# Kernel optimization log

Hardware: AMD Instinct MI355X
Metric: run time of the kernel (lower is better)

The kernel has to match this reference:

```python
import jax, jax.numpy as jnp
from jax import lax
import numpy as np

D = 1024      # d_model
H = 16        # n_heads == n_v_heads
DK = 64       # head_k_dim = d_model // n_heads
DV = 128      # head_v_dim = head_dim * expand_v (2.0)
KDIM = H * DK   # 1024
VDIM = H * DV   # 2048
CONV_K = 4
B, T = 2, 4096
EPS = 1e-5


def setup_inputs() -> dict:
    key = jax.random.key(0)
    ks = jax.random.split(key, 14)
    def w(k, shape, s=0.02):
        return jax.random.normal(k, shape, jnp.float32) * s
    return {
        "x": jax.random.normal(ks[0], (B, T, D), jnp.float32),
        "w_q": w(ks[1], (D, KDIM)),
        "w_k": w(ks[2], (D, KDIM)),
        "w_v": w(ks[3], (D, VDIM)),
        "w_a": w(ks[4], (D, H)),
        "w_b": w(ks[5], (D, H)),
        "w_g": w(ks[6], (D, VDIM)),
        "w_out": w(ks[7], (VDIM, D)),
        "A_log": jnp.log(jax.random.uniform(ks[8], (H,), jnp.float32, 1.0, 16.0)),
        "dt_bias": jax.random.uniform(ks[9], (H,), jnp.float32, -4.0, -1.0),
        "conv_q": w(ks[10], (KDIM, CONV_K), 0.1),
        "conv_k": w(ks[11], (KDIM, CONV_K), 0.1),
        "conv_v": w(ks[12], (VDIM, CONV_K), 0.1),
        "norm_w": jnp.ones((DV,), jnp.float32),
    }


def _causal_conv_silu(x, w):
    # x: [B,T,C], w: [C,Kw]  depthwise causal conv1d followed by SiLU
    C = x.shape[-1]
    Kw = w.shape[-1]
    xp = jnp.pad(x, ((0, 0), (Kw - 1, 0), (0, 0))).transpose(0, 2, 1)  # [B,C,T+Kw-1]
    y = lax.conv_general_dilated(
        xp, w[:, None, :], window_strides=(1,), padding="VALID",
        feature_group_count=C, dimension_numbers=("NCH", "OIH", "NCH"))
    return jax.nn.silu(y.transpose(0, 2, 1))  # [B,T,C]


def _l2norm(x, eps=1e-6):
    return x * lax.rsqrt(jnp.sum(x * x, axis=-1, keepdims=True) + eps)


def _gated_delta_rule(q, k, v, g, beta):
    # q,k: [B,T,H,DK] (l2-normalized), v: [B,T,H,DV], g,beta: [B,T,H]
    scale = q.shape[-1] ** -0.5
    qs = jnp.moveaxis(q, 1, 0)
    ks_ = jnp.moveaxis(k, 1, 0)
    vs = jnp.moveaxis(v, 1, 0)
    gs = jnp.moveaxis(g, 1, 0)
    bs = jnp.moveaxis(beta, 1, 0)

    def step(S, inp):
        q_t, k_t, v_t, g_t, b_t = inp
        S = S * jnp.exp(g_t)[..., None, None]            # gated decay
        mem = jnp.einsum("bhk,bhkv->bhv", k_t, S)        # current memory readout
        delta = (v_t - mem) * b_t[..., None]             # beta-weighted delta
        S = S + jnp.einsum("bhk,bhv->bhkv", k_t, delta)  # delta-rule update
        o_t = jnp.einsum("bhk,bhkv->bhv", q_t * scale, S)
        return S, o_t

    S0 = jnp.zeros((q.shape[0], q.shape[2], q.shape[3], v.shape[3]), q.dtype)
    _, o = lax.scan(step, S0, (qs, ks_, vs, gs, bs))
    return jnp.moveaxis(o, 0, 1)  # [B,T,H,DV]


def reference(x, w_q, w_k, w_v, w_a, w_b, w_g, w_out, A_log, dt_bias,
              conv_q, conv_k, conv_v, norm_w):
    Bx, Tx, _ = x.shape
    q = x @ w_q
    k = x @ w_k
    v = x @ w_v
    beta = jax.nn.sigmoid(x @ w_b) * 2.0                      # allow_neg_eigval
    g = -jnp.exp(A_log) * jax.nn.softplus((x @ w_a) + dt_bias)  # [B,T,H]

    q = _causal_conv_silu(q, conv_q)
    k = _causal_conv_silu(k, conv_k)
    v = _causal_conv_silu(v, conv_v)

    q = q.reshape(Bx, Tx, H, DK)
    k = k.reshape(Bx, Tx, H, DK)
    v = v.reshape(Bx, Tx, H, DV)

    # use_qk_l2norm_in_kernel=True
    q = _l2norm(q)
    k = _l2norm(k)

    o = _gated_delta_rule(q, k, v, g, beta)  # [B,T,H,DV]

    # gated RMSNorm: normalize o, gate with silu(w_g(x))
    g_gate = (x @ w_g).reshape(Bx, Tx, H, DV)
    rms = o * lax.rsqrt(jnp.mean(o * o, axis=-1, keepdims=True) + EPS)
    y = rms * norm_w * jax.nn.silu(g_gate)
    return y.reshape(Bx, Tx, VDIM) @ w_out
```

## Files before the change

kernel.cpp:

```cpp
#include <hip/hip_runtime.h>
#include <hip/hip_bf16.h>
#include <math.h>

#define Bc 2
#define Tc 4096
#define Dc 1024
#define Hc 16
#define DKc 64
#define DVc 128
#define KDIMc 1024
#define VDIMc 2048
#define Mrows (Bc*Tc)
#define CC 64
#define NCH (Tc/CC)

typedef short short8 __attribute__((ext_vector_type(8)));
typedef float f32x4 __attribute__((ext_vector_type(4)));

__device__ __forceinline__ float siluf(float x) {
    return x / (1.f + __expf(-x));
}
__device__ __forceinline__ float dot4(float4 a, float4 b) {
    return a.x * b.x + a.y * b.y + a.z * b.z + a.w * b.w;
}
__device__ __forceinline__ unsigned short f2bf(float f) {
    unsigned int u = __float_as_uint(f);
    unsigned int r = (u + 0x7fffu + ((u >> 16) & 1u)) >> 16;
    return (unsigned short)r;
}
__device__ __forceinline__ unsigned int pk2(float a, float b) {
    return (unsigned)f2bf(a) | ((unsigned)f2bf(b) << 16);
}
__device__ __forceinline__ float bf2f(unsigned short s) {
    unsigned int u = ((unsigned int)s) << 16;
    return __uint_as_float(u);
}
__device__ __forceinline__ void gload16(const unsigned short* g,
                                        unsigned short* l) {
    __builtin_amdgcn_global_load_lds(
        (const __attribute__((address_space(1))) unsigned int*)g,
        (__attribute__((address_space(3))) unsigned int*)l, 16, 0, 0);
}

__device__ void tile_transp_bf16(const float* __restrict__ in,
                                 unsigned short* __restrict__ out, int K,
                                 int N, int blk) {
    __shared__ float t[32][33];
    const int nbx = N >> 5;
    const int n0 = (blk % nbx) << 5;
    const int k0 = (blk / nbx) << 5;
    const int c = threadIdx.x & 31, r4 = (threadIdx.x >> 5) << 2;
#pragma unroll
    for (int i = 0; i < 4; i++)
        t[r4 + i][c] = in[(size_t)(k0 + r4 + i) * N + n0 + c];
    __syncthreads();
#pragma unroll
    for (int i = 0; i < 4; i++)
        out[(size_t)(n0 + r4 + i) * K + k0 + c] = f2bf(t[c][r4 + i]);
}

__device__ void tile_transp_f32w(const float* __restrict__ in,
                                 float* __restrict__ out, int blk) {
    __shared__ float t2[64][17];
    const int k0 = blk * 64;
    const int r = threadIdx.x >> 2, c4 = (threadIdx.x & 3) << 2;
    float4 v = *(const float4*)&in[(size_t)(k0 + r) * 16 + c4];
    t2[r][c4 + 0] = v.x;
    t2[r][c4 + 1] = v.y;
    t2[r][c4 + 2] = v.z;
    t2[r][c4 + 3] = v.w;
    __syncthreads();
    const int n = threadIdx.x >> 4;
    const int kk = (threadIdx.x & 15) << 2;
    out[(size_t)n * Dc + k0 + kk + 0] = t2[kk + 0][n];
    out[(size_t)n * Dc + k0 + kk + 1] = t2[kk + 1][n];
    out[(size_t)n * Dc + k0 + kk + 2] = t2[kk + 2][n];
    out[(size_t)n * Dc + k0 + kk + 3] = t2[kk + 3][n];
}

__global__ void __launch_bounds__(256) prep_all(
    const float* __restrict__ x, const float* __restrict__ w_q,
    const float* __restrict__ w_k, const float* __restrict__ w_v,
    const float* __restrict__ w_g, const float* __restrict__ w_out,
    const float* __restrict__ w_a, const float* __restrict__ w_b,
    unsigned short* __restrict__ xb, unsigned short* __restrict__ wqT,
    unsigned short* __restrict__ wkT, unsigned short* __restrict__ wvT,
    unsigned short* __restrict__ wgT, unsigned short* __restrict__ woT,
    float* __restrict__ waT, float* __restrict__ wbT) {
    int blk = blockIdx.x;
    if (blk < 1024) { tile_transp_bf16(w_q, wqT, Dc, KDIMc, blk); return; }
    blk -= 1024;
    if (blk < 1024) { tile_transp_bf16(w_k, wkT, Dc, KDIMc, blk); return; }
    blk -= 1024;
    if (blk < 2048) { tile_transp_bf16(w_v, wvT, Dc, VDIMc, blk); return; }
    blk -= 2048;
    if (blk < 2048) { tile_transp_bf16(w_g, wgT, Dc, VDIMc, blk); return; }
    blk -= 2048;
    if (blk < 2048) { tile_transp_bf16(w_out, woT, VDIMc, Dc, blk); return; }
    blk -= 2048;
    if (blk < 16) { tile_transp_f32w(w_a, waT, blk); return; }
    blk -= 16;
    if (blk < 16) { tile_transp_f32w(w_b, wbT, blk); return; }
    blk -= 16;
    int g = blk * 256 + threadIdx.x;
    float4 v = *(const float4*)&x[(size_t)g * 4];
    *(uint2*)&xb[(size_t)g * 4] = make_uint2(pk2(v.x, v.y), pk2(v.z, v.w));
}

__global__ void __launch_bounds__(256) transp_k16(
    const unsigned short* __restrict__ in, unsigned short* __restrict__ out) {
    __shared__ unsigned short t[64][68];
    const int bx = blockIdx.x & 63;
    const int by = (blockIdx.x >> 6) & 15;
    const int b = blockIdx.x >> 10;
    const int t0 = bx << 6, c0 = by << 6;
    {
        const int row = threadIdx.x >> 2, c16 = (threadIdx.x & 3) << 4;
        const unsigned short* src =
            &in[((size_t)b * Tc + t0 + row) * KDIMc + c0 + c16];
#pragma unroll
        for (int i = 0; i < 4; i++)
            *(uint2*)&t[row][c16 + i * 4] = *(const uint2*)&src[i * 4];
    }
    __syncthreads();
    {
        const int cc = threadIdx.x & 63, tp = (threadIdx.x >> 6) << 4;
        unsigned short v[16];
#pragma unroll
        for (int i = 0; i < 16; i++) v[i] = t[tp + i][cc];
        unsigned short* dst =
            &out[((size_t)b * KDIMc + c0 + cc) * Tc + t0 + tp];
        *(uint4*)&dst[0] = *(uint4*)&v[0];
        *(uint4*)&dst[8] = *(uint4*)&v[8];
    }
}

#define GEMM_SHARED()                                                         \
    __shared__ unsigned short As0[128 * 32], As1[128 * 32];                   \
    __shared__ unsigned short Bs0[128 * 32], Bs1[128 * 32];

#define GEMM_STAGE64(Ap, Bp, Kk)                                              \
    {                                                                         \
        const size_t kb0 = (size_t)(kt << 6) + gcol;                          \
        const size_t kb1 = kb0 + 32;                                          \
        _Pragma("unroll") for (int r = 0; r < 2; r++) {                       \
            const int rows = r * 64 + w * 16;                                 \
            gload16(&Ap[(size_t)(m0 + rows + grow) * Kk + kb0],               \
                    &As0[rows * 32]);                                         \
            gload16(&Ap[(size_t)(m0 + rows + grow) * Kk + kb1],               \
                    &As1[rows * 32]);                                         \
            gload16(&Bp[(size_t)(n0 + rows + grow) * Kk + kb0],               \
                    &Bs0[rows * 32]);                                         \
            gload16(&Bp[(size_t)(n0 + rows + grow) * Kk + kb1],               \
                    &Bs1[rows * 32]);                                         \
        }                                                                     \
    }

#define GEMM_MFMA64()                                                         \
    {                                                                         \
        short8 af[4], bfr[4];                                                 \
        _Pragma("unroll") for (int i = 0; i < 4; i++)                         \
            af[i] = *(const short8*)&As0[(wr + i * 16 + fr) * 32 + fk8];      \
        _Pragma("unroll") for (int j = 0; j < 4; j++)                         \
            bfr[j] = *(const short8*)&Bs0[(wc + j * 16 + fr) * 32 + fk8];     \
        _Pragma("unroll") for (int i = 0; i < 4; i++)                         \
            _Pragma("unroll") for (int j = 0; j < 4; j++)                     \
                acc[i][j] = __builtin_amdgcn_mfma_f32_16x16x32_bf16(          \
                    af[i], bfr[j], acc[i][j], 0, 0, 0);                       \
        _Pragma("unroll") for (int i = 0; i < 4; i++)                         \
            af[i] = *(const short8*)&As1[(wr + i * 16 + fr) * 32 + fk8];      \
        _Pragma("unroll") for (int j = 0; j < 4; j++)                         \
            bfr[j] = *(const short8*)&Bs1[(wc + j * 16 + fr) * 32 + fk8];     \
        _Pragma("unroll") for (int i = 0; i < 4; i++)                         \
            _Pragma("unroll") for (int j = 0; j < 4; j++)                     \
                acc[i][j] = __builtin_amdgcn_mfma_f32_16x16x32_bf16(          \
                    af[i], bfr[j], acc[i][j], 0, 0, 0);                       \
    }

#define GEMM_KLOOP(Ap, Bp, Kk)                                                \
    {                                                                         \
        const int nkt = (Kk) >> 6;                                            \
        for (int kt = 0; kt < nkt; kt++) {                                    \
            __syncthreads();                                                  \
            GEMM_STAGE64(Ap, Bp, Kk);                                         \
            __syncthreads();                                                  \
            GEMM_MFMA64();                                                    \
        }                                                                     \
    }

__global__ void __launch_bounds__(256) gemm_qkv(
    const unsigned short* __restrict__ A, const unsigned short* __restrict__ Bt,
    unsigned short* __restrict__ q16, unsigned short* __restrict__ k16,
    float* __restrict__ vb) {
    GEMM_SHARED();
    const int tid = threadIdx.x;
    const int bx = blockIdx.x & 31, by = blockIdx.x >> 5;
    const int m0 = by << 7, n0 = bx << 7;
    const int w = tid >> 6, lane = tid & 63;
    const int wr = (w >> 1) << 6, wc = (w & 1) << 6;
    const int fr = lane & 15, fk8 = (lane >> 4) << 3;
    const int grow = lane >> 2;
    const int gcol = (lane & 3) << 3;

    f32x4 acc[4][4];
#pragma unroll
    for (int i = 0; i < 4; i++)
#pragma unroll
        for (int j = 0; j < 4; j++)
            acc[i][j] = (f32x4){0.f, 0.f, 0.f, 0.f};

    GEMM_KLOOP(A, Bt, Dc);

    const int cr = (lane >> 4) << 2;
    if (bx < 16) {
        unsigned short* Cb = (bx < 8) ? q16 : k16;
        const int coloff = (bx & 7) << 7;
#pragma unroll
        for (int i = 0; i < 4; i++)
#pragma unroll
            for (int j = 0; j < 4; j++) {
#pragma unroll
                for (int r = 0; r < 4; r++) {
                    Cb[(size_t)(m0 + wr + i * 16 + cr + r) * KDIMc + coloff +
                       wc + j * 16 + fr] = f2bf(acc[i][j][r]);
                }
            }
    } else {
        const int coloff = (bx - 16) << 7;
#pragma unroll
        for (int i = 0; i < 4; i++)
#pragma unroll
            for (int j = 0; j < 4; j++) {
#pragma unroll
                for (int r = 0; r < 4; r++) {
                    vb[(size_t)(m0 + wr + i * 16 + cr + r) * VDIMc + coloff +
                       wc + j * 16 + fr] = acc[i][j][r];
                }
            }
    }
}

__global__ void __launch_bounds__(256) gemm_bf16(
    const unsigned short* __restrict__ A, const unsigned short* __restrict__ Bt,
    float* __restrict__ C, int M, int N, int K) {
    GEMM_SHARED();
    const int tid = threadIdx.x;
    const int nbx = N >> 7;
    const int bx = blockIdx.x % nbx, by = blockIdx.x / nbx;
    const int m0 = by << 7, n0 = bx << 7;
    const int w = tid >> 6, lane = tid & 63;
    const int wr = (w >> 1) << 6, wc = (w & 1) << 6;
    const int fr = lane & 15, fk8 = (lane >> 4) << 3;
    const int grow = lane >> 2;
    const int gcol = (lane & 3) << 3;

    f32x4 acc[4][4];
#pragma unroll
    for (int i = 0; i < 4; i++)
#pragma unroll
        for (int j = 0; j < 4; j++)
            acc[i][j] = (f32x4){0.f, 0.f, 0.f, 0.f};

    GEMM_KLOOP(A, Bt, K);

    const int cr = (lane >> 4) << 2;
#pragma unroll
    for (int i = 0; i < 4; i++)
#pragma unroll
        for (int j = 0; j < 4; j++) {
#pragma unroll
            for (int r = 0; r < 4; r++) {
                C[(size_t)(m0 + wr + i * 16 + cr + r) * N + n0 + wc + j * 16 +
                  fr] = acc[i][j][r];
            }
        }
}

__global__ void __launch_bounds__(256) gemm_gate_rms(
    const unsigned short* __restrict__ A, const unsigned short* __restrict__ Bt,
    const unsigned short* __restrict__ o, const float* __restrict__ rfac,
    const float* __restrict__ norm_w, unsigned short* __restrict__ out,
    int M, int N, int K) {
    GEMM_SHARED();
    const int tid = threadIdx.x;
    const int nbx = N >> 7;
    const int bx = blockIdx.x % nbx, by = blockIdx.x / nbx;
    const int m0 = by << 7, n0 = bx << 7;
    const int h = n0 >> 7;
    const int w = tid >> 6, lane = tid & 63;
    const int wr = (w >> 1) << 6, wc = (w & 1) << 6;
    const int fr = lane & 15, fk8 = (lane >> 4) << 3;
    const int grow = lane >> 2;
    const int gcol = (lane & 3) << 3;

    f32x4 acc[4][4];
#pragma unroll
    for (int i = 0; i < 4; i++)
#pragma unroll
        for (int j = 0; j < 4; j++)
            acc[i][j] = (f32x4){0.f, 0.f, 0.f, 0.f};

    GEMM_KLOOP(A, Bt, K);

    const int cr = (lane >> 4) << 2;
#pragma unroll
    for (int i = 0; i < 4; i++)
#pragma unroll
        for (int j = 0; j < 4; j++) {
            const int colh = wc + j * 16 + fr;
            const float nw = norm_w[colh];
#pragma unroll
            for (int r = 0; r < 4; r++) {
                const int row = m0 + wr + i * 16 + cr + r;
                float ov = bf2f(o[(size_t)row * VDIMc + n0 + colh]);
                float f = rfac[(size_t)row * Hc + h];
                float y = ov * f * nw * siluf(acc[i][j][r]);
                out[(size_t)row * VDIMc + n0 + colh] = f2bf(y);
            }
        }
}

__global__ void __launch_bounds__(256) rfac_kernel(
    const unsigned short* __restrict__ o, float* __restrict__ rf) {
    const int row = blockIdx.x * 4 + (threadIdx.x >> 6);
    const int lane = threadIdx.x & 63;
    const size_t base = (size_t)row * DVc;
    unsigned int pv = *(const unsigned int*)&o[base + lane * 2];
    float o0 = bf2f((unsigned short)(pv & 0xffff));
    float o1 = bf2f((unsigned short)(pv >> 16));
    float ss = o0 * o0 + o1 * o1;
#pragma unroll
    for (int m = 1; m < 64; m <<= 1) ss += __shfl_xor(ss, m, 64);
    if (lane == 0) rf[row] = rsqrtf(ss * (1.f / 128.f) + 1e-5f);
}

__global__ void __launch_bounds__(256) ab_proj(
    const float* __restrict__ x, const float* __restrict__ w_aT,
    const float* __restrict__ w_bT, const float* __restrict__ A_log,
    const float* __restrict__ dt_bias, float* __restrict__ g_out,
    float* __restrict__ beta_out) {
    const int wv = threadIdx.x >> 6;
    const int lane = threadIdx.x & 63;
    const int h = lane >> 2, kg = lane & 3;
    const int row0 = blockIdx.x * 16 + wv * 4;
    const float* wa = w_aT + (size_t)h * Dc + kg * 256;
    const float* wb = w_bT + (size_t)h * Dc + kg * 256;
    const float* xr = x + (size_t)row0 * Dc + kg * 256;
    float pa[4] = {0.f, 0.f, 0.f, 0.f}, pb[4] = {0.f, 0.f, 0.f, 0.f};
#pragma unroll 4
    for (int k = 0; k < 256; k += 4) {
        float4 a4 = *(const float4*)&wa[k];
        float4 b4 = *(const float4*)&wb[k];
#pragma unroll
        for (int r = 0; r < 4; r++) {
            float4 x4 = *(const float4*)&xr[(size_t)r * Dc + k];
            pa[r] += dot4(x4, a4);
            pb[r] += dot4(x4, b4);
        }
    }
#pragma unroll
    for (int r = 0; r < 4; r++) {
        pa[r] += __shfl_xor(pa[r], 1, 64);
        pa[r] += __shfl_xor(pa[r], 2, 64);
        pb[r] += __shfl_xor(pb[r], 1, 64);
        pb[r] += __shfl_xor(pb[r], 2, 64);
    }
    if (kg == 0) {
        const float el = __expf(A_log[h]);
        const float db = dt_bias[h];
#pragma unroll
        for (int r = 0; r < 4; r++) {
            float arg = pa[r] + db;
            float sp = fmaxf(arg, 0.f) + log1pf(__expf(-fabsf(arg)));
            g_out[(size_t)(row0 + r) * Hc + h] = -el * sp;
            beta_out[(size_t)(row0 + r) * Hc + h] =
                2.f / (1.f + __expf(-pb[r]));
        }
    }
}

template <int C>
__global__ void __launch_bounds__(256) save_halo(
    const float* __restrict__ in, float* __restrict__ halo) {
    const int g = blockIdx.x * 256 + threadIdx.x;
    const int total = Bc * (Tc / 64 - 1) * 3 * C;
    if (g >= total) return;
    const int c = g % C;
    int r = g / C;
    const int j = r % 3;
    r /= 3;
    const int chunk = r % (Tc / 64 - 1) + 1;
    const int b = r / (Tc / 64 - 1);
    halo[((size_t)(b * 64 + chunk) * 3 + j) * C + c] =
        in[((size_t)b * Tc + chunk * 64 - 3 + j) * C + c];
}

__global__ void __launch_bounds__(256) conv_qk(
    const unsigned short* __restrict__ qin, const float* __restrict__ wq,
    unsigned short* __restrict__ qout, const unsigned short* __restrict__ kin,
    const float* __restrict__ wk, unsigned short* __restrict__ kout) {
    constexpr int C = KDIMc;
    constexpr int CB = C / 256;
    const int half = Bc * (Tc / 64) * CB;
    int bidx = blockIdx.x;
    const unsigned short* in;
    const float* w;
    unsigned short* out;
    if (bidx < half) { in = qin; w = wq; out = qout; }
    else { bidx -= half; in = kin; w = wk; out = kout; }
    const int cb = bidx % CB;
    const int tchunk = (bidx / CB) % (Tc / 64);
    const int b = bidx / (CB * (Tc / 64));
    const int c = cb * 256 + threadIdx.x;
    const int t0 = tchunk * 64;
    const float w0 = w[c * 4 + 0], w1 = w[c * 4 + 1], w2 = w[c * 4 + 2],
                w3 = w[c * 4 + 3];
    const unsigned short* src = in + (size_t)b * Tc * C + c;
    float xm3 = (t0 >= 3) ? bf2f(src[(size_t)(t0 - 3) * C]) : 0.f;
    float xm2 = (t0 >= 2) ? bf2f(src[(size_t)(t0 - 2) * C]) : 0.f;
    float xm1 = (t0 >= 1) ? bf2f(src[(size_t)(t0 - 1) * C]) : 0.f;
    unsigned short* dst = out + (size_t)b * Tc * C + c;
#pragma unroll 4
    for (int i = 0; i < 64; i++) {
        float xt = bf2f(src[(size_t)(t0 + i) * C]);
        float y = w0 * xm3 + w1 * xm2 + w2 * xm1 + w3 * xt;
        y = siluf(y);
        {
            float ss = y * y;
#pragma unroll
            for (int m = 1; m < 64; m <<= 1) ss += __shfl_xor(ss, m, 64);
            y *= rsqrtf(ss + 1e-6f);
        }
        dst[(size_t)(t0 + i) * C] = f2bf(y);
        xm3 = xm2;
        xm2 = xm1;
        xm1 = xt;
    }
}

template <int C, bool L2N>
__global__ void __launch_bounds__(256) conv_silu_inplace(
    float* __restrict__ buf, const float* __restrict__ w,
    const float* __restrict__ halo) {
    constexpr int CB = C / 256;
    const int bidx = blockIdx.x;
    const int cb = bidx % CB;
    const int tchunk = (bidx / CB) % (Tc / 64);
    const int b = bidx / (CB * (Tc / 64));
    const int c = cb * 256 + threadIdx.x;
    const int t0 = tchunk * 64;
    const float w0 = w[c * 4 + 0], w1 = w[c * 4 + 1], w2 = w[c * 4 + 2],
                w3 = w[c * 4 + 3];
    float xm3 = 0.f, xm2 = 0.f, xm1 = 0.f;
    if (tchunk > 0) {
        const float* hp = halo + (size_t)(b * 64 + tchunk) * 3 * C + c;
        xm3 = hp[0];
        xm2 = hp[C];
        xm1 = hp[2 * C];
    }
    float* p = buf + (size_t)b * Tc * C + c;
#pragma unroll 4
    for (int i = 0; i < 64; i++) {
        float xt = p[(size_t)(t0 + i) * C];
        float y = w0 * xm3 + w1 * xm2 + w2 * xm1 + w3 * xt;
        y = siluf(y);
        if (L2N) {
            float ss = y * y;
#pragma unroll
            for (int m = 1; m < 64; m <<= 1) ss += __shfl_xor(ss, m, 64);
            y *= rsqrtf(ss + 1e-6f);
        }
        p[(size_t)(t0 + i) * C] = y;
        xm3 = xm2;
        xm2 = xm1;
        xm1 = xt;
    }
}

__global__ void __launch_bounds__(256) tm_precompute(
    const unsigned short* __restrict__ kc, const unsigned short* __restrict__ qc,
    const float* __restrict__ g, const float* __restrict__ beta,
    unsigned short* __restrict__ tmT, unsigned short* __restrict__ tmM) {
    const int bid = blockIdx.x;
    const int ch = bid & (NCH - 1);
    const int bh = bid >> 6;
    const int b = bh >> 4, h = bh & 15;
    const int tid = threadIdx.x;
    const int t0 = ch * CC;

    __shared__ __align__(16) unsigned short kb16[CC][72];
    __shared__ __align__(16) unsigned short qb16[CC][72];
    __shared__ __align__(16) float AtL[CC][DKc + 4];
    __shared__ float cL[CC], betaL[CC];

    const size_t qk0 = (size_t)b * Tc * KDIMc + h * DKc;
    const size_t gb0 = (size_t)b * Tc * Hc + h;
    const size_t tile = (size_t)(bh * NCH + ch) * 4096;

#pragma unroll
    for (int i = 0; i < 2; i++) {
        int e = tid + i * 256;
        int r = e >> 3, c8 = (e & 7) << 3;
        *(short8*)&kb16[r][c8] =
            *(const short8*)&kc[qk0 + (size_t)(t0 + r) * KDIMc + c8];
        *(short8*)&qb16[r][c8] =
            *(const short8*)&qc[qk0 + (size_t)(t0 + r) * KDIMc + c8];
    }
    if (tid < 64) {
        float gv = g[gb0 + (size_t)(t0 + tid) * Hc];
        float cv = gv;
#pragma unroll
        for (int d = 1; d < 64; d <<= 1) {
            float nb = __shfl_up(cv, d, 64);
            if (tid >= d) cv += nb;
        }
        cL[tid] = cv;
        betaL[tid] = beta[gb0 + (size_t)(t0 + tid) * Hc];
    }
    __syncthreads();

    {
        const int w = tid >> 6, lane = tid & 63;
        const int fr = lane & 15, fk8 = (lane >> 4) << 3;
        const int rr = (lane >> 4) << 2;
        short8 ak0 = *(const short8*)&kb16[w * 16 + fr][fk8];
        short8 ak1 = *(const short8*)&kb16[w * 16 + fr][fk8 + 32];
        short8 aq0 = *(const short8*)&qb16[w * 16 + fr][fk8];
        short8 aq1 = *(const short8*)&qb16[w * 16 + fr][fk8 + 32];
#pragma unroll
        for (int j = 0; j < 4; j++) {
            short8 b0 = *(const short8*)&kb16[j * 16 + fr][fk8];
            short8 b1 = *(const short8*)&kb16[j * 16 + fr][fk8 + 32];
            f32x4 kk = (f32x4){0.f, 0.f, 0.f, 0.f};
            f32x4 qk = (f32x4){0.f, 0.f, 0.f, 0.f};
            kk = __builtin_amdgcn_mfma_f32_16x16x32_bf16(ak0, b0, kk, 0, 0, 0);
            kk = __builtin_amdgcn_mfma_f32_16x16x32_bf16(ak1, b1, kk, 0, 0, 0);
            qk = __builtin_amdgcn_mfma_f32_16x16x32_bf16(aq0, b0, qk, 0, 0, 0);
            qk = __builtin_amdgcn_mfma_f32_16x16x32_bf16(aq1, b1, qk, 0, 0, 0);
#pragma unroll
            for (int r = 0; r < 4; r++) {
                int t = w * 16 + rr + r, s = j * 16 + fr;
                float E = (s <= t) ? __expf(cL[t] - cL[s]) : 0.f;
                AtL[s][t] = (s < t) ? betaL[t] * E * kk[r] : 0.f;
                tmM[tile + (size_t)t * 64 + s] =
                    (s <= t) ? f2bf(0.125f * E * qk[r]) : (unsigned short)0;
            }
        }
    }
    __syncthreads();

    {
        const int w = tid >> 6, lane = tid & 63;
        float acc[16];
#pragma unroll
        for (int di = 0; di < 16; di++)
            acc[di] = (lane == w * 16 + di) ? 1.f : 0.f;
#pragma unroll
        for (int s = 0; s < 64; s++) {
            float a = AtL[s][lane];
            float ds[16];
#pragma unroll
            for (int di = 0; di < 16; di++)
                ds[di] = __uint_as_float(
                    __builtin_amdgcn_readlane(__float_as_uint(acc[di]), s));
#pragma unroll
            for (int di = 0; di < 16; di++)
                acc[di] = fmaf(-a, ds[di], acc[di]);
        }
        unsigned short tb[16];
#pragma unroll
        for (int di = 0; di < 16; di++) tb[di] = f2bf(acc[di]);
        *(uint4*)&tmT[tile + (size_t)lane * 64 + w * 16] = *(uint4*)&tb[0];
        *(uint4*)&tmT[tile + (size_t)lane * 64 + w * 16 + 8] = *(uint4*)&tb[8];
    }
}

__global__ void __launch_bounds__(512, 2) delta_scan(
    const unsigned short* __restrict__ kc, const unsigned short* __restrict__ qc,
    const unsigned short* __restrict__ kcT,
    const float* __restrict__ vc, unsigned short* __restrict__ o16,
    const float* __restrict__ g, const float* __restrict__ beta,
    const unsigned short* __restrict__ tmT,
    const unsigned short* __restrict__ tmM) {
    const int bid = blockIdx.x;
    const int sl = bid >> 5;
    const int bh = bid & 31;
    const int b = bh >> 4, h = bh & 15;
    const int tid = threadIdx.x;

    __shared__ __align__(16) float VL[CC][20];
    __shared__ float gamL[CC], egL[CC], betaL[CC];
    __shared__ __align__(16) unsigned short kb16[CC][72];
    __shared__ __align__(16) unsigned short kh16[CC][72];
    __shared__ __align__(16) unsigned short qb16[CC][72];
    __shared__ __align__(16) unsigned short Tb16[CC][72];
    __shared__ __align__(16) unsigned short Mb16[CC][72];
    __shared__ __align__(16) unsigned short STb16[16][72];
    __shared__ __align__(16) unsigned short DTb16[16][72];
    __shared__ __align__(16) unsigned short D2b16[16][72];
    __shared__ __align__(16) unsigned short egd16[16][72];

    const size_t qk0 = (size_t)b * Tc * KDIMc + h * DKc;
    const size_t kT0 = ((size_t)b * KDIMc + h * DKc) * Tc;
    const size_t v0 = (size_t)b * Tc * VDIMc + h * DVc + sl * 16;
    const size_t gb0 = (size_t)b * Tc * Hc + h;
    const size_t tb0 = (size_t)(bh * NCH) * 4096;

    for (int i = tid; i < 16 * 72; i += 512) ((unsigned short*)STb16)[i] = 0;

    const int r8 = tid >> 3, c8 = (tid & 7) << 3;
    const int wid = tid >> 6, lane = tid & 63;
    const int fr = lane & 15;
    const int fk8 = (lane >> 4) << 3;
    const int rr = (lane >> 4) << 2;

    f32x4 accS = (f32x4){0.f, 0.f, 0.f, 0.f};

    short8 kv, kvT, qv, tv, mv;
    float4 vv0;
    float gvr = 0.f, bvr = 0.f;

#define LOADREGS(CH)                                                          \
    {                                                                         \
        const size_t tK = qk0 + (size_t)(CH) * CC * KDIMc;                    \
        const size_t tile_ = tb0 + (size_t)(CH) * 4096;                       \
        kv = *(const short8*)&kc[tK + (size_t)r8 * KDIMc + c8];               \
        kvT = *(const short8*)&kcT[kT0 + (size_t)r8 * Tc + (CH) * CC + c8];   \
        qv = *(const short8*)&qc[tK + (size_t)r8 * KDIMc + c8];               \
        tv = *(const short8*)&tmT[tile_ + (size_t)tid * 8];                   \
        mv = *(const short8*)&tmM[tile_ + (size_t)tid * 8];                   \
        if (tid < 256)                                                        \
            vv0 = *(const float4*)&vc[v0 +                                    \
                                      (size_t)((CH) * CC + (tid >> 2)) *     \
                                          VDIMc +                             \
                                      ((tid & 3) << 2)];                      \
        if (tid < 64) {                                                       \
            gvr = g[gb0 + (size_t)((CH) * CC + tid) * Hc];                    \
            bvr = beta[gb0 + (size_t)((CH) * CC + tid) * Hc];                 \
        }                                                                     \
    }

    LOADREGS(0);

#pragma unroll 1
    for (int ch = 0; ch < NCH; ch++) {
        __syncthreads();

        {
            *(short8*)&kb16[r8][c8] = kv;
            *(short8*)&kh16[r8][c8] = kvT;
            *(short8*)&qb16[r8][c8] = qv;
            *(short8*)&Tb16[r8][c8] = tv;
            *(short8*)&Mb16[r8][c8] = mv;
            if (tid < 256) *(float4*)&VL[tid >> 2][(tid & 3) << 2] = vv0;
            if (tid < 64) {
                float cv = gvr;
#pragma unroll
                for (int d = 1; d < 64; d <<= 1) {
                    float nb = __shfl_up(cv, d, 64);
                    if (tid >= d) cv += nb;
                }
                gamL[tid] = __expf(cv);
                float cend = __shfl(cv, 63, 64);
                egL[tid] = __expf(cend - cv);
                betaL[tid] = bvr;
            }
        }
        if (ch + 1 < NCH) LOADREGS(ch + 1);
        __syncthreads();

        f32x4 acc1 = (f32x4){0.f, 0.f, 0.f, 0.f};
        {
            short8 bs0 = *(const short8*)&STb16[fr][fk8];
            short8 bs1 = *(const short8*)&STb16[fr][fk8 + 32];
            if (wid < 4) {
                const int m0 = wid << 4;
                short8 a0 = *(const short8*)&kb16[m0 + fr][fk8];
                short8 a1 = *(const short8*)&kb16[m0 + fr][fk8 + 32];
                acc1 = __builtin_amdgcn_mfma_f32_16x16x32_bf16(a0, bs0, acc1, 0, 0, 0);
                acc1 = __builtin_amdgcn_mfma_f32_16x16x32_bf16(a1, bs1, acc1, 0, 0, 0);
#pragma unroll
                for (int r = 0; r < 4; r++) {
                    int t = m0 + rr + r;
                    float rhs = betaL[t] * (VL[t][fr] - gamL[t] * acc1[r]);
                    DTb16[fr][t] = f2bf(rhs);
                }
            } else {
                const int m0 = (wid - 4) << 4;
                short8 a0 = *(const short8*)&qb16[m0 + fr][fk8];
                short8 a1 = *(const short8*)&qb16[m0 + fr][fk8 + 32];
                acc1 = __builtin_amdgcn_mfma_f32_16x16x32_bf16(a0, bs0, acc1, 0, 0, 0);
                acc1 = __builtin_amdgcn_mfma_f32_16x16x32_bf16(a1, bs1, acc1, 0, 0, 0);
#pragma unroll
                for (int r = 0; r < 4; r++) {
                    int t = m0 + rr + r;
                    acc1[r] *= 0.125f * gamL[t];
                }
            }
        }
        __syncthreads();

        if (wid < 4) {
            const int m0 = wid << 4;
            short8 a0 = *(const short8*)&Tb16[m0 + fr][fk8];
            short8 a1 = *(const short8*)&Tb16[m0 + fr][fk8 + 32];
            short8 b0 = *(const short8*)&DTb16[fr][fk8];
            short8 b1 = *(const short8*)&DTb16[fr][fk8 + 32];
            f32x4 d = (f32x4){0.f, 0.f, 0.f, 0.f};
            d = __builtin_amdgcn_mfma_f32_16x16x32_bf16(a0, b0, d, 0, 0, 0);
            d = __builtin_amdgcn_mfma_f32_16x16x32_bf16(a1, b1, d, 0, 0, 0);
#pragma unroll
            for (int r = 0; r < 4; r++) {
                int t = m0 + rr + r;
                D2b16[fr][t] = f2bf(d[r]);
                egd16[fr][t] = f2bf(egL[t] * d[r]);
            }
        }
        __syncthreads();

        if (wid >= 4) {
            const int m0 = (wid - 4) << 4;
            short8 a0 = *(const short8*)&Mb16[m0 + fr][fk8];
            short8 a1 = *(const short8*)&Mb16[m0 + fr][fk8 + 32];
            short8 b0 = *(const short8*)&D2b16[fr][fk8];
            short8 b1 = *(const short8*)&D2b16[fr][fk8 + 32];
            f32x4 o = acc1;
            o = __builtin_amdgcn_mfma_f32_16x16x32_bf16(a0, b0, o, 0, 0, 0);
            o = __builtin_amdgcn_mfma_f32_16x16x32_bf16(a1, b1, o, 0, 0, 0);
#pragma unroll
            for (int r = 0; r < 4; r++)
                o16[v0 + (size_t)(ch * CC + m0 + rr + r) * VDIMc + fr] =
                    f2bf(o[r]);
        } else {
            const int m0 = wid << 4;
            const float ge = gamL[63];
            short8 a0 = *(const short8*)&kh16[m0 + fr][fk8];
            short8 a1 = *(const short8*)&kh16[m0 + fr][fk8 + 32];
            short8 b0 = *(const short8*)&egd16[fr][fk8];
            short8 b1 = *(const short8*)&egd16[fr][fk8 + 32];
#pragma unroll
            for (int r = 0; r < 4; r++) accS[r] *= ge;
            accS = __builtin_amdgcn_mfma_f32_16x16x32_bf16(a0, b0, accS, 0, 0, 0);
            accS = __builtin_amdgcn_mfma_f32_16x16x32_bf16(a1, b1, accS, 0, 0, 0);
#pragma unroll
            for (int r = 0; r < 4; r++)
                STb16[fr][m0 + rr + r] = f2bf(accS[r]);
        }
    }
#undef LOADREGS
}

extern "C" void kernel_launch(void* const* d_in, const int* in_sizes, int n_in,
                              void* d_out, int out_size, void* d_ws,
                              size_t ws_size, hipStream_t stream) {
    const float* x = (const float*)d_in[0];
    const float* w_q = (const float*)d_in[1];
    const float* w_k = (const float*)d_in[2];
    const float* w_v = (const float*)d_in[3];
    const float* w_a = (const float*)d_in[4];
    const float* w_b = (const float*)d_in[5];
    const float* w_g = (const float*)d_in[6];
    const float* w_out = (const float*)d_in[7];
    const float* A_log = (const float*)d_in[8];
    const float* dt_bias = (const float*)d_in[9];
    const float* conv_q = (const float*)d_in[10];
    const float* conv_k = (const float*)d_in[11];
    const float* conv_v = (const float*)d_in[12];
    const float* norm_w = (const float*)d_in[13];

    float* ws = (float*)d_ws;
    const size_t M = Mrows;
    float* qb = ws;
    float* kb = qb + M * KDIMc;
    float* vb = kb + M * KDIMc;
    float* tm = vb + M * VDIMc;
    float* gbuf = tm + M * VDIMc;
    float* bbuf = gbuf + M * Hc;
    float* xtra = bbuf + M * Hc;

    unsigned short* q16raw = (unsigned short*)qb;
    unsigned short* k16raw = (unsigned short*)kb;
    unsigned short* kcT16 = (unsigned short*)qb;
    unsigned short* o16 = (unsigned short*)kb;
    unsigned short* tmS = (unsigned short*)tm;
    unsigned short* tmT16 = tmS;
    unsigned short* tmM16 = tmS + (size_t)8388608;
    unsigned short* qc16 = tmS + (size_t)16777216;
    unsigned short* kc16 = tmS + (size_t)25165824;
    float* halo = tm;
    unsigned short* obb = tmS;
    float* rfac = gbuf;

    unsigned short* xb = (unsigned short*)xtra;
    unsigned short* wqT = xb + M * KDIMc;
    unsigned short* wkT = wqT + (size_t)KDIMc * Dc;
    unsigned short* wvT = wkT + (size_t)KDIMc * Dc;
    unsigned short* wgT = wvT + (size_t)VDIMc * Dc;
    unsigned short* woT = wgT + (size_t)VDIMc * Dc;
    float* waT = (float*)(woT + (size_t)Dc * VDIMc);
    float* wbT = waT + (size_t)16 * Dc;

    prep_all<<<dim3(1024 + 1024 + 2048 + 2048 + 2048 + 16 + 16 + 8192), 256,
               0, stream>>>(x, w_q, w_k, w_v, w_g, w_out, w_a, w_b, xb, wqT,
                            wkT, wvT, wgT, woT, waT, wbT);

    gemm_qkv<<<dim3((M / 128) * 32), 256, 0, stream>>>(xb, wqT, q16raw, k16raw,
                                                       vb);

    ab_proj<<<dim3(M / 16), 256, 0, stream>>>(x, waT, wbT, A_log, dt_bias,
                                              gbuf, bbuf);

    conv_qk<<<dim3(2 * Bc * (Tc / 64) * (KDIMc / 256)), 256, 0, stream>>>(
        q16raw, conv_q, qc16, k16raw, conv_k, kc16);
    transp_k16<<<dim3(Bc * 16 * 64), 256, 0, stream>>>(kc16, kcT16);
    {
        const int nv = Bc * (Tc / 64 - 1) * 3 * VDIMc;
        save_halo<VDIMc><<<dim3((nv + 255) / 256), 256, 0, stream>>>(vb, halo);
        conv_silu_inplace<VDIMc, false>
            <<<dim3(Bc * (Tc / 64) * (VDIMc / 256)), 256, 0, stream>>>(
                vb, conv_v, halo);
    }

    tm_precompute<<<dim3(Bc * Hc * NCH), 256, 0, stream>>>(
        kc16, qc16, gbuf, bbuf, tmT16, tmM16);
    delta_scan<<<dim3(Bc * Hc * 8), 512, 0, stream>>>(
        kc16, qc16, kcT16, vb, o16, gbuf, bbuf, tmT16, tmM16);

    rfac_kernel<<<dim3(M * Hc / 4), 256, 0, stream>>>(o16, rfac);
    gemm_gate_rms<<<dim3((M / 128) * (VDIMc / 128)), 256, 0, stream>>>(
        xb, wgT, o16, rfac, norm_w, obb, M, VDIMc, Dc);

    gemm_bf16<<<dim3((M / 128) * (Dc / 128)), 256, 0, stream>>>(
        obb, woT, (float*)d_out, M, Dc, VDIMc);
}
```

Before: 496.6 us.

## Double-buffer GEMM shared-memory tiles to overlap global loads with MFMA

Doubles the shared-memory A/B tile buffers and restructures the shared GEMM K-loop so the next K-tile is fetched into the alternate buffer while MFMAs run on the current one. This drops one barrier per iteration and is meant to hide global-load latency behind compute. In exchange, shared memory per block doubles, which may reduce how many blocks fit on each CU.

```diff
diff --git a/kernel.cpp b/kernel.cpp
--- a/kernel.cpp
+++ b/kernel.cpp
@@ -136,41 +136,41 @@
 }
 
 #define GEMM_SHARED()                                                         \
-    __shared__ unsigned short As0[128 * 32], As1[128 * 32];                   \
-    __shared__ unsigned short Bs0[128 * 32], Bs1[128 * 32];
-
-#define GEMM_STAGE64(Ap, Bp, Kk)                                              \
+    __shared__ unsigned short As0[2][128 * 32], As1[2][128 * 32];             \
+    __shared__ unsigned short Bs0[2][128 * 32], Bs1[2][128 * 32];
+
+#define GEMM_STAGE64(Ap, Bp, Kk, KT, PB)                                      \
     {                                                                         \
-        const size_t kb0 = (size_t)(kt << 6) + gcol;                          \
+        const size_t kb0 = (size_t)((KT) << 6) + gcol;                        \
         const size_t kb1 = kb0 + 32;                                          \
         _Pragma("unroll") for (int r = 0; r < 2; r++) {                       \
             const int rows = r * 64 + w * 16;                                 \
             gload16(&Ap[(size_t)(m0 + rows + grow) * Kk + kb0],               \
-                    &As0[rows * 32]);                                         \
+                    &As0[PB][rows * 32]);                                     \
             gload16(&Ap[(size_t)(m0 + rows + grow) * Kk + kb1],               \
-                    &As1[rows * 32]);                                         \
+                    &As1[PB][rows * 32]);                                     \
             gload16(&Bp[(size_t)(n0 + rows + grow) * Kk + kb0],               \
-                    &Bs0[rows * 32]);                                         \
+                    &Bs0[PB][rows * 32]);                                     \
             gload16(&Bp[(size_t)(n0 + rows + grow) * Kk + kb1],               \
-                    &Bs1[rows * 32]);                                         \
+                    &Bs1[PB][rows * 32]);                                     \
         }                                                                     \
     }
 
-#define GEMM_MFMA64()                                                         \
+#define GEMM_MFMA64(PB)                                                       \
     {                                                                         \
         short8 af[4], bfr[4];                                                 \
         _Pragma("unroll") for (int i = 0; i < 4; i++)                         \
-            af[i] = *(const short8*)&As0[(wr + i * 16 + fr) * 32 + fk8];      \
+            af[i] = *(const short8*)&As0[PB][(wr + i * 16 + fr) * 32 + fk8];  \
         _Pragma("unroll") for (int j = 0; j < 4; j++)                         \
-            bfr[j] = *(const short8*)&Bs0[(wc + j * 16 + fr) * 32 + fk8];     \
+            bfr[j] = *(const short8*)&Bs0[PB][(wc + j * 16 + fr) * 32 + fk8]; \
         _Pragma("unroll") for (int i = 0; i < 4; i++)                         \
             _Pragma("unroll") for (int j = 0; j < 4; j++)                     \
                 acc[i][j] = __builtin_amdgcn_mfma_f32_16x16x32_bf16(          \
                     af[i], bfr[j], acc[i][j], 0, 0, 0);                       \
         _Pragma("unroll") for (int i = 0; i < 4; i++)                         \
-            af[i] = *(const short8*)&As1[(wr + i * 16 + fr) * 32 + fk8];      \
+            af[i] = *(const short8*)&As1[PB][(wr + i * 16 + fr) * 32 + fk8];  \
         _Pragma("unroll") for (int j = 0; j < 4; j++)                         \
-            bfr[j] = *(const short8*)&Bs1[(wc + j * 16 + fr) * 32 + fk8];     \
+            bfr[j] = *(const short8*)&Bs1[PB][(wc + j * 16 + fr) * 32 + fk8]; \
         _Pragma("unroll") for (int i = 0; i < 4; i++)                         \
             _Pragma("unroll") for (int j = 0; j < 4; j++)                     \
                 acc[i][j] = __builtin_amdgcn_mfma_f32_16x16x32_bf16(          \
@@ -180,12 +180,16 @@
 #define GEMM_KLOOP(Ap, Bp, Kk)                                                \
     {                                                                         \
         const int nkt = (Kk) >> 6;                                            \
-        for (int kt = 0; kt < nkt; kt++) {                                    \
-            __syncthreads();                                                  \
-            GEMM_STAGE64(Ap, Bp, Kk);                                         \
-            __syncthreads();                                                  \
-            GEMM_MFMA64();                                                    \
+        GEMM_STAGE64(Ap, Bp, Kk, 0, 0);                                       \
+        __syncthreads();                   \
+        int cur = 0;                                                          \
+        for (int kt = 0; kt < nkt - 1; kt++) {                                \
+            GEMM_STAGE64(Ap, Bp, Kk, kt + 1, cur ^ 1);    \
+            GEMM_MFMA64(cur);                            \
+            __syncthreads();            \
+            cur ^= 1;                                                         \
         }                                                                     \
+        GEMM_MFMA64(cur);                                      \
     }
 
 __global__ void __launch_bounds__(256) gemm_qkv(
```

Result: slower. 524.3 us (+5.6%).
